# Optimization experiments

Hardware: AMD Instinct MI355X
Metric: run time of the kernel (lower is better)

Reference implementation:

```python
import jax, jax.numpy as jnp
import numpy as np

SHAPES = [(100, 100), (50, 50), (25, 25), (13, 13)]
EMBED, HEADS, LEVELS, POINTS = 256, 8, 4, 4
DH = EMBED // HEADS


def setup_inputs() -> dict:
    key = jax.random.key(0)
    ks = jax.random.split(key, 12)
    bs, nq = 4, 10000
    nv = sum(h * w for h, w in SHAPES)
    s = 0.02
    return {
        'query': jax.random.normal(ks[0], (bs, nq, EMBED), jnp.float32),
        'value': jax.random.normal(ks[1], (bs, nv, EMBED), jnp.float32),
        'reference_points': jax.random.uniform(ks[2], (bs, nq, LEVELS, 2), jnp.float32),
        'spatial_shapes': jnp.array(SHAPES, jnp.int32),
        'Wv': s * jax.random.normal(ks[3], (EMBED, EMBED), jnp.float32),
        'bv': jnp.zeros((EMBED,), jnp.float32),
        'Woff': s * jax.random.normal(ks[4], (EMBED, HEADS * LEVELS * POINTS * 2), jnp.float32),
        'boff': s * jax.random.normal(ks[5], (HEADS * LEVELS * POINTS * 2,), jnp.float32),
        'Ww': s * jax.random.normal(ks[6], (EMBED, HEADS * LEVELS * POINTS), jnp.float32),
        'bw': jnp.zeros((HEADS * LEVELS * POINTS,), jnp.float32),
        'Wo': s * jax.random.normal(ks[7], (EMBED, EMBED), jnp.float32),
        'bo': jnp.zeros((EMBED,), jnp.float32),
    }


def _msda(v, loc, aw, bs, nq):
    # v: (bs, nv, heads, dh); loc: (bs, nq, heads, L, P, 2) normalized in [0,1]
    # aw: (bs, nq, heads, L, P). Bilinear grid_sample, align_corners=False, zero padding.
    out = jnp.zeros((bs, HEADS, nq, DH), v.dtype)
    start = 0
    for l, (H, W) in enumerate(SHAPES):
        vl = v[:, start:start + H * W].transpose(0, 2, 1, 3)  # (bs, heads, H*W, dh)
        start += H * W
        locl = loc[:, :, :, l]                                # (bs, nq, heads, P, 2)
        x = locl[..., 0] * W - 0.5                            # align_corners=False mapping
        y = locl[..., 1] * H - 0.5
        x0 = jnp.floor(x); y0 = jnp.floor(y)
        fx = x - x0; fy = y - y0
        x0i = x0.astype(jnp.int32); y0i = y0.astype(jnp.int32)
        sampled = jnp.zeros((bs, HEADS, nq * POINTS, DH), v.dtype)
        for dy, wy in ((0, 1.0 - fy), (1, fy)):
            for dx, wx in ((0, 1.0 - fx), (1, fx)):
                xi = x0i + dx; yi = y0i + dy
                valid = (xi >= 0) & (xi < W) & (yi >= 0) & (yi < H)
                idx = jnp.clip(yi, 0, W and H - 1) * W + jnp.clip(xi, 0, W - 1)
                idx = jnp.clip(yi, 0, H - 1) * W + jnp.clip(xi, 0, W - 1)
                idx_t = idx.transpose(0, 2, 1, 3).reshape(bs, HEADS, nq * POINTS)
                g = jnp.take_along_axis(vl, idx_t[..., None], axis=2)  # (bs,heads,nq*P,dh)
                w = jnp.where(valid, wx * wy, 0.0).transpose(0, 2, 1, 3).reshape(bs, HEADS, -1)
                sampled = sampled + g * w[..., None]
        awl = aw[:, :, :, l].transpose(0, 2, 1, 3).reshape(bs, HEADS, nq * POINTS)
        out = out + (sampled * awl[..., None]).reshape(bs, HEADS, nq, POINTS, DH).sum(3)
    return out.transpose(0, 2, 1, 3).reshape(bs, nq, EMBED)


def reference(query, value, reference_points, spatial_shapes, Wv, bv, Woff, boff, Ww, bw, Wo, bo):
    bs, nq, _ = query.shape
    v = (value @ Wv + bv).reshape(bs, -1, HEADS, DH)
    off = (query @ Woff + boff).reshape(bs, nq, HEADS, LEVELS, POINTS, 2)
    aw = jax.nn.softmax((query @ Ww + bw).reshape(bs, nq, HEADS, LEVELS * POINTS), axis=-1)
    aw = aw.reshape(bs, nq, HEADS, LEVELS, POINTS)
    normalizer = jnp.stack([spatial_shapes[:, 1], spatial_shapes[:, 0]], -1).astype(query.dtype)  # (L,2) = (W,H)
    loc = reference_points[:, :, None, :, None, :] + off / normalizer[None, None, None, :, None, :]
    out = _msda(v, loc, aw, bs, nq)
    out = out @ Wo + bo
    return out + query  # identity residual (dropout in eval mode)
```

## Files before the change

### kernel.cpp

```cpp
#include <hip/hip_runtime.h>
#include <hip/hip_bf16.h>

#define BS     4
#define NQ     10000
#define NV     13294
#define EMBED  256
#define HEADS  8
#define LEVELS 4
#define POINTS 4
#define DH     32

typedef __attribute__((ext_vector_type(8))) short short8;
typedef __attribute__((ext_vector_type(4))) float floatx4;

static __device__ __forceinline__ unsigned short f2b(float f) {
    __hip_bfloat16 h = __float2bfloat16(f);
    return *(unsigned short*)&h;
}
static __device__ __forceinline__ float b2f(unsigned short u) {
    return __uint_as_float(((unsigned int)u) << 16);
}
static __device__ __forceinline__ unsigned int pk_bf16(float x, float y) {
    __hip_bfloat162 h = __float22bfloat162_rn(make_float2(x, y));
    unsigned int u; __builtin_memcpy(&u, &h, 4); return u;
}

__global__ __launch_bounds__(256) void prep_weights(
    const float* __restrict__ Wv,  const float* __restrict__ Woff,
    const float* __restrict__ boff,const float* __restrict__ Ww,
    const float* __restrict__ bw,  const float* __restrict__ Wo,
    unsigned short* __restrict__ Wvt, unsigned short* __restrict__ Wcatt,
    unsigned short* __restrict__ Wot, float* __restrict__ bcat)
{
    const int n = blockIdx.x;
    const int k = threadIdx.x;
    if (n < 256) {
        Wvt[n * 256 + k] = f2b(Wv[k * 256 + n]);
    } else if (n < 512) {
        Wcatt[(n - 256) * 256 + k] = f2b(Woff[k * 256 + (n - 256)]);
    } else if (n < 640) {
        Wcatt[(n - 256) * 256 + k] = f2b(Ww[k * 128 + (n - 512)]);
    } else {
        Wot[(n - 640) * 256 + k] = f2b(Wo[k * 256 + (n - 640)]);
    }
    if (n == 0) {
        for (int j = k; j < 384; j += 256)
            bcat[j] = (j < 256) ? boff[j] : bw[j - 256];
    }
}

#define ASTR 72

template<int MODE, bool AF32>
static __device__ __forceinline__ void gemm_body(
    unsigned short* As, unsigned short* Bsh,
    const void* __restrict__ Aptr, int M,
    const unsigned short* __restrict__ Bt,
    const float* __restrict__ bias,
    void* __restrict__ Cv, int ldc,
    const float* __restrict__ residual,
    int mb, int nb)
{
    const int t  = threadIdx.x;
    const int m0 = mb * 128;
    const int n0 = nb * 128;
    const int K  = 256;

    const int wv   = t >> 6;
    const int lane = t & 63;
    const int wm   = (wv & 1) * 64;
    const int wn   = (wv >> 1) * 64;
    const int lr   = lane & 15;
    const int lk   = (lane >> 4) * 8;

    floatx4 acc[4][4] = {};

    const int ar = t >> 1;
    const int ac = (t & 1) * 32;

    for (int k0 = 0; k0 < K; k0 += 64) {
        uint4 a[4] = {{}, {}, {}, {}};
        const int arow = m0 + ar;
        if (AF32) {
            if (arow < M) {
                const float4* s = (const float4*)((const float*)Aptr + (size_t)arow * K + k0 + ac);
                #pragma unroll
                for (int i = 0; i < 4; ++i) {
                    const float4 f0 = s[2 * i], f1 = s[2 * i + 1];
                    a[i].x = pk_bf16(f0.x, f0.y);
                    a[i].y = pk_bf16(f0.z, f0.w);
                    a[i].z = pk_bf16(f1.x, f1.y);
                    a[i].w = pk_bf16(f1.z, f1.w);
                }
            }
        } else {
            if (arow < M) {
                const uint4* s = (const uint4*)((const unsigned short*)Aptr + (size_t)arow * K + k0 + ac);
                a[0] = s[0]; a[1] = s[1]; a[2] = s[2]; a[3] = s[3];
            }
        }
        const uint4* bs = (const uint4*)(Bt + (size_t)(n0 + ar) * K + k0 + ac);
        const uint4 b0 = bs[0], b1 = bs[1], b2 = bs[2], b3 = bs[3];

        __syncthreads();
        {
            uint4* ad = (uint4*)&As[ar * ASTR + ac];
            ad[0] = a[0]; ad[1] = a[1]; ad[2] = a[2]; ad[3] = a[3];
            uint4* bd = (uint4*)&Bsh[ar * ASTR + ac];
            bd[0] = b0; bd[1] = b1; bd[2] = b2; bd[3] = b3;
        }
        __syncthreads();

        #pragma unroll
        for (int kk = 0; kk < 64; kk += 32) {
            short8 bf[4];
            #pragma unroll
            for (int nt = 0; nt < 4; ++nt)
                bf[nt] = *(const short8*)&Bsh[(wn + nt * 16 + lr) * ASTR + kk + lk];
            #pragma unroll
            for (int mt = 0; mt < 4; ++mt) {
                const short8 af = *(const short8*)&As[(wm + mt * 16 + lr) * ASTR + kk + lk];
                #pragma unroll
                for (int nt = 0; nt < 4; ++nt)
                    acc[mt][nt] = __builtin_amdgcn_mfma_f32_16x16x32_bf16(af, bf[nt], acc[mt][nt], 0, 0, 0);
            }
        }
    }

    const int rbase = m0 + wm + (lane >> 4) * 4;
    #pragma unroll
    for (int nt = 0; nt < 4; ++nt) {
        const int col = n0 + wn + nt * 16 + lr;
        const float bb = bias[col];
        #pragma unroll
        for (int mt = 0; mt < 4; ++mt) {
            #pragma unroll
            for (int r = 0; r < 4; ++r) {
                const int row = rbase + mt * 16 + r;
                if (row < M) {
                    float val = acc[mt][nt][r] + bb;
                    if (MODE == 2) val += residual[(size_t)row * ldc + col];
                    if (MODE == 0)
                        ((unsigned short*)Cv)[(size_t)row * ldc + col] = f2b(val);
                    else
                        ((float*)Cv)[(size_t)row * ldc + col] = val;
                }
            }
        }
    }
}

__global__ __launch_bounds__(256) void gemm_fused12(
    const float* __restrict__ value, const float* __restrict__ query,
    const unsigned short* __restrict__ Wvt, const unsigned short* __restrict__ Wcatt,
    const float* __restrict__ bv, const float* __restrict__ bcat,
    unsigned short* __restrict__ vout, unsigned short* __restrict__ projout)
{
    __shared__ __align__(16) unsigned short As[128 * ASTR];
    __shared__ __align__(16) unsigned short Bsh[128 * ASTR];
    const unsigned int bid = blockIdx.x;
    if (bid < 832u) {
        gemm_body<0, true>(As, Bsh, value, BS * NV, Wvt, bv, vout, 256, nullptr,
                           (int)(bid >> 1), (int)(bid & 1));
    } else {
        const unsigned int b2 = bid - 832u;
        gemm_body<0, true>(As, Bsh, query, BS * NQ, Wcatt, bcat, projout, 384, nullptr,
                           (int)(b2 / 3u), (int)(b2 % 3u));
    }
}

__global__ __launch_bounds__(256) void gemm_out(
    const unsigned short* __restrict__ msda, const unsigned short* __restrict__ Wot,
    const float* __restrict__ bo, float* __restrict__ out,
    const float* __restrict__ query)
{
    __shared__ __align__(16) unsigned short As[128 * ASTR];
    __shared__ __align__(16) unsigned short Bsh[128 * ASTR];
    gemm_body<2, false>(As, Bsh, msda, BS * NQ, Wot, bo, out, 256, query,
                        (int)blockIdx.x, (int)blockIdx.y);
}

__global__ __launch_bounds__(256) void msda_sample(
    const unsigned short* __restrict__ v,
    const unsigned short* __restrict__ proj,
    const float* __restrict__ rp,
    unsigned short* __restrict__ out)
{
    __shared__ __align__(16) unsigned int taps[4 * 1056];

    const int wave = threadIdx.x >> 6;
    const int lane = threadIdx.x & 63;
    const int q = blockIdx.x * 4 + wave;
    const int b = blockIdx.y;
    const int rowq = b * NQ + q;
    const unsigned short* prow = proj + (size_t)rowq * 384;

    const int hA = lane >> 3;
    const int li = lane & 7;
    const int c0 = li * 2;

    const ushort2 lgu = *(const ushort2*)&prow[256 + hA * 16 + c0];
    const float lgx = b2f(lgu.x), lgy = b2f(lgu.y);
    float mx = fmaxf(lgx, lgy);
    mx = fmaxf(mx, __shfl_xor(mx, 1));
    mx = fmaxf(mx, __shfl_xor(mx, 2));
    mx = fmaxf(mx, __shfl_xor(mx, 4));
    const float e0 = __expf(lgx - mx);
    const float e1 = __expf(lgy - mx);
    float ssum = e0 + e1;
    ssum += __shfl_xor(ssum, 1);
    ssum += __shfl_xor(ssum, 2);
    ssum += __shfl_xor(ssum, 4);
    const float inv = 1.0f / ssum;

    const int l = c0 >> 2;
    const int Wl = (l == 0) ? 100 : (l == 1) ? 50 : (l == 2) ? 25 : 13;
    const int st = (l == 0) ? 0 : (l == 1) ? 10000 : (l == 2) ? 12500 : 13125;
    const int Hl = Wl;
    const float fW = (float)Wl, fH = (float)Hl;

    const float2 rxy = *(const float2*)&rp[((size_t)rowq * 4 + l) * 2];

    unsigned int* tbase = taps + wave * 1056 + hA * 132;

    #pragma unroll
    for (int cc = 0; cc < 2; ++cc) {
        const int c = c0 + cc;
        const ushort2 oxyu = *(const ushort2*)&prow[hA * 32 + c * 2];
        const float ox = b2f(oxyu.x), oy = b2f(oxyu.y);
        const float aww = (cc ? e1 : e0) * inv;
        const float x = fmaf(rxy.x, fW, ox) - 0.5f;
        const float y = fmaf(rxy.y, fH, oy) - 0.5f;
        const float x0f = floorf(x), y0f = floorf(y);
        const float fx = x - x0f, fy = y - y0f;
        const int ix = (int)x0f, iy = (int)y0f;
        const float wxv[2] = {1.f - fx, fx};
        const float wyv[2] = {1.f - fy, fy};

        uint4 ent[2];
        #pragma unroll
        for (int tp = 0; tp < 4; ++tp) {
            const int dy = tp >> 1, dx = tp & 1;
            const int xi = ix + dx, yi = iy + dy;
            const bool ok = (xi >= 0) && (xi < Wl) && (yi >= 0) && (yi < Hl);
            const int cx = min(max(xi, 0), Wl - 1);
            const int cy = min(max(yi, 0), Hl - 1);
            const unsigned int off = (unsigned int)(st + cy * Wl + cx) * 512u + (unsigned int)hA * 64u;
            const float w = ok ? wyv[dy] * wxv[dx] * aww : 0.f;
            ((unsigned int*)&ent[tp >> 1])[(tp & 1) * 2 + 0] = off;
            ((unsigned int*)&ent[tp >> 1])[(tp & 1) * 2 + 1] = __float_as_uint(w);
        }
        *(uint4*)&tbase[(c * 4 + 0) * 2] = ent[0];
        *(uint4*)&tbase[(c * 4 + 2) * 2] = ent[1];
    }

    __syncthreads();

    const int h = lane >> 3;
    const unsigned int lane_off = (unsigned int)(lane & 7) * 8u;
    const char* vbase = (const char*)v + (size_t)b * NV * 512;
    const uint4* tp4 = (const uint4*)(taps + wave * 1056 + h * 132);

    float a0 = 0.f, a1 = 0.f, a2 = 0.f, a3 = 0.f;
    #pragma unroll 8
    for (int j = 0; j < 32; ++j) {
        const uint4 ee = tp4[j];
        const uint2 g0 = *(const uint2*)(vbase + (ee.x + lane_off));
        const uint2 g1 = *(const uint2*)(vbase + (ee.z + lane_off));
        const float w0 = __uint_as_float(ee.y);
        const float w1 = __uint_as_float(ee.w);
        a0 = fmaf(w0, __uint_as_float(g0.x << 16), a0);
        a1 = fmaf(w0, __uint_as_float(g0.x & 0xFFFF0000u), a1);
        a2 = fmaf(w0, __uint_as_float(g0.y << 16), a2);
        a3 = fmaf(w0, __uint_as_float(g0.y & 0xFFFF0000u), a3);
        a0 = fmaf(w1, __uint_as_float(g1.x << 16), a0);
        a1 = fmaf(w1, __uint_as_float(g1.x & 0xFFFF0000u), a1);
        a2 = fmaf(w1, __uint_as_float(g1.y << 16), a2);
        a3 = fmaf(w1, __uint_as_float(g1.y & 0xFFFF0000u), a3);
    }

    ushort4 o;
    o.x = f2b(a0); o.y = f2b(a1); o.z = f2b(a2); o.w = f2b(a3);
    *(ushort4*)&out[(size_t)rowq * 256 + h * 32 + (lane & 7) * 4] = o;
}

extern "C" void kernel_launch(void* const* d_in, const int* in_sizes, int n_in,
                              void* d_out, int out_size, void* d_ws, size_t ws_size,
                              hipStream_t stream) {
    const float* query = (const float*)d_in[0];
    const float* value = (const float*)d_in[1];
    const float* rp    = (const float*)d_in[2];
    const float* Wv    = (const float*)d_in[4];
    const float* bv    = (const float*)d_in[5];
    const float* Woff  = (const float*)d_in[6];
    const float* boff  = (const float*)d_in[7];
    const float* Ww    = (const float*)d_in[8];
    const float* bw    = (const float*)d_in[9];
    const float* Wo    = (const float*)d_in[10];
    const float* bo    = (const float*)d_in[11];
    float* out = (float*)d_out;

    const int Mv = BS * NV;
    const int Mq = BS * NQ;

    char* ws = (char*)d_ws;
    const size_t SZ_MSDA = (size_t)Mq * 256 * 2;
    const size_t SZ_V    = (size_t)Mv * 256 * 2;
    const size_t SZ_PROJ = (size_t)Mq * 384 * 2;
    unsigned short* msda  = (unsigned short*)(ws);
    unsigned short* v_bf  = (unsigned short*)(ws + SZ_MSDA);
    unsigned short* proj  = (unsigned short*)(ws + SZ_MSDA + SZ_V);
    char* wp = ws + SZ_MSDA + SZ_V + SZ_PROJ;
    unsigned short* Wvt   = (unsigned short*)(wp);
    unsigned short* Wcatt = (unsigned short*)(wp + 256 * 256 * 2);
    unsigned short* Wot   = (unsigned short*)(wp + 256 * 256 * 2 + 384 * 256 * 2);
    float*          bcat  = (float*)(wp + 256 * 256 * 2 + 384 * 256 * 2 + 256 * 256 * 2);

    prep_weights<<<896, 256, 0, stream>>>(Wv, Woff, boff, Ww, bw, Wo, Wvt, Wcatt, Wot, bcat);

    gemm_fused12<<<832 + 939, 256, 0, stream>>>(
        value, query, Wvt, Wcatt, bv, bcat, v_bf, proj);

    msda_sample<<<dim3(NQ / 4, BS), 256, 0, stream>>>(v_bf, proj, rp, msda);

    gemm_out<<<dim3((Mq + 127) / 128, 2), 256, 0, stream>>>(msda, Wot, bo, out, query);
}
```

Baseline: 332.7 us.

## Load GEMM operands directly from global memory into MFMA registers, dropping LDS staging

The GEMM body no longer stages A and B tiles through shared memory with barriers. Each wave now loads its MFMA fragments straight from global memory (converting fp32 A to bf16 in registers) and clamps out-of-range rows instead of zero-filling them. This removes LDS traffic and __syncthreads, which may raise occupancy. The cost is redundant global/L2 reads, since the two waves sharing a column range each reload B and the two sharing a row range each reload A, with less coalesced access.

After: 356.8 us. +7.2%, slower.

```diff
diff --git a/kernel.cpp b/kernel.cpp
--- a/kernel.cpp
+++ b/kernel.cpp
@@ -49,11 +49,8 @@
     }
 }
 
-#define ASTR 72
-
 template<int MODE, bool AF32>
-static __device__ __forceinline__ void gemm_body(
-    unsigned short* As, unsigned short* Bsh,
+static __device__ __forceinline__ void gemm_direct(
     const void* __restrict__ Aptr, int M,
     const unsigned short* __restrict__ Bt,
     const float* __restrict__ bias,
@@ -61,76 +58,57 @@
     const float* __restrict__ residual,
     int mb, int nb)
 {
-    const int t  = threadIdx.x;
-    const int m0 = mb * 128;
-    const int n0 = nb * 128;
-    const int K  = 256;
-
+    const int t    = threadIdx.x;
+    const int lane = t & 63;
     const int wv   = t >> 6;
-    const int lane = t & 63;
-    const int wm   = (wv & 1) * 64;
-    const int wn   = (wv >> 1) * 64;
+    const int wm   = mb * 128 + (wv & 1) * 64;
+    const int wn   = nb * 128 + (wv >> 1) * 64;
     const int lr   = lane & 15;
     const int lk   = (lane >> 4) * 8;
 
     floatx4 acc[4][4] = {};
 
-    const int ar = t >> 1;
-    const int ac = (t & 1) * 32;
-
-    for (int k0 = 0; k0 < K; k0 += 64) {
-        uint4 a[4] = {{}, {}, {}, {}};
-        const int arow = m0 + ar;
-        if (AF32) {
-            if (arow < M) {
-                const float4* s = (const float4*)((const float*)Aptr + (size_t)arow * K + k0 + ac);
-                #pragma unroll
-                for (int i = 0; i < 4; ++i) {
-                    const float4 f0 = s[2 * i], f1 = s[2 * i + 1];
-                    a[i].x = pk_bf16(f0.x, f0.y);
-                    a[i].y = pk_bf16(f0.z, f0.w);
-                    a[i].z = pk_bf16(f1.x, f1.y);
-                    a[i].w = pk_bf16(f1.z, f1.w);
-                }
-            }
-        } else {
-            if (arow < M) {
-                const uint4* s = (const uint4*)((const unsigned short*)Aptr + (size_t)arow * K + k0 + ac);
-                a[0] = s[0]; a[1] = s[1]; a[2] = s[2]; a[3] = s[3];
+    int arow[4];
+    #pragma unroll
+    for (int mt = 0; mt < 4; ++mt)
+        arow[mt] = min(wm + mt * 16 + lr, M - 1);
+
+    #pragma unroll 2
+    for (int k0 = 0; k0 < 256; k0 += 32) {
+        short8 bf[4];
+        #pragma unroll
+        for (int nt = 0; nt < 4; ++nt)
+            bf[nt] = *(const short8*)&Bt[(size_t)(wn + nt * 16 + lr) * 256 + k0 + lk];
+
+        short8 af[4];
+        #pragma unroll
+        for (int mt = 0; mt < 4; ++mt) {
+            if (AF32) {
+                const float4* s = (const float4*)((const float*)Aptr + (size_t)arow[mt] * 256 + k0 + lk);
+                const float4 f0 = s[0], f1 = s[1];
+                union { short8 v; unsigned int u[4]; } cv;
+                cv.u[0] = pk_bf16(f0.x, f0.y);
+                cv.u[1] = pk_bf16(f0.z, f0.w);
+                cv.u[2] = pk_bf16(f1.x, f1.y);
+                cv.u[3] = pk_bf16(f1.z, f1.w);
+                af[mt] = cv.v;
+            } else {
+                af[mt] = *(const short8*)&((const unsigned short*)Aptr)[(size_t)arow[mt] * 256 + k0 + lk];
             }
         }
-        const uint4* bs = (const uint4*)(Bt + (size_t)(n0 + ar) * K + k0 + ac);
-        const uint4 b0 = bs[0], b1 = bs[1], b2 = bs[2], b3 = bs[3];
-
-        __syncthreads();
-        {
-            uint4* ad = (uint4*)&As[ar * ASTR + ac];
-            ad[0] = a[0]; ad[1] = a[1]; ad[2] = a[2]; ad[3] = a[3];
-            uint4* bd = (uint4*)&Bsh[ar * ASTR + ac];
-            bd[0] = b0; bd[1] = b1; bd[2] = b2; bd[3] = b3;
-        }
-        __syncthreads();
-
-        #pragma unroll
-        for (int kk = 0; kk < 64; kk += 32) {
-            short8 bf[4];
+
+        #pragma unroll
+        for (int mt = 0; mt < 4; ++mt) {
             #pragma unroll
             for (int nt = 0; nt < 4; ++nt)
-                bf[nt] = *(const short8*)&Bsh[(wn + nt * 16 + lr) * ASTR + kk + lk];
-            #pragma unroll
-            for (int mt = 0; mt < 4; ++mt) {
-                const short8 af = *(const short8*)&As[(wm + mt * 16 + lr) * ASTR + kk + lk];
-                #pragma unroll
-                for (int nt = 0; nt < 4; ++nt)
-                    acc[mt][nt] = __builtin_amdgcn_mfma_f32_16x16x32_bf16(af, bf[nt], acc[mt][nt], 0, 0, 0);
-            }
+                acc[mt][nt] = __builtin_amdgcn_mfma_f32_16x16x32_bf16(af[mt], bf[nt], acc[mt][nt], 0, 0, 0);
         }
     }
 
-    const int rbase = m0 + wm + (lane >> 4) * 4;
+    const int rbase = wm + (lane >> 4) * 4;
     #pragma unroll
     for (int nt = 0; nt < 4; ++nt) {
-        const int col = n0 + wn + nt * 16 + lr;
+        const int col = wn + nt * 16 + lr;
         const float bb = bias[col];
         #pragma unroll
         for (int mt = 0; mt < 4; ++mt) {
@@ -156,16 +134,14 @@
     const float* __restrict__ bv, const float* __restrict__ bcat,
     unsigned short* __restrict__ vout, unsigned short* __restrict__ projout)
 {
-    __shared__ __align__(16) unsigned short As[128 * ASTR];
-    __shared__ __align__(16) unsigned short Bsh[128 * ASTR];
     const unsigned int bid = blockIdx.x;
     if (bid < 832u) {
-        gemm_body<0, true>(As, Bsh, value, BS * NV, Wvt, bv, vout, 256, nullptr,
-                           (int)(bid >> 1), (int)(bid & 1));
+        gemm_direct<0, true>(value, BS * NV, Wvt, bv, vout, 256, nullptr,
+                             (int)(bid >> 1), (int)(bid & 1));
     } else {
         const unsigned int b2 = bid - 832u;
-        gemm_body<0, true>(As, Bsh, query, BS * NQ, Wcatt, bcat, projout, 384, nullptr,
-                           (int)(b2 / 3u), (int)(b2 % 3u));
+        gemm_direct<0, true>(query, BS * NQ, Wcatt, bcat, projout, 384, nullptr,
+                             (int)(b2 / 3u), (int)(b2 % 3u));
     }
 }
 
@@ -174,10 +150,8 @@
     const float* __restrict__ bo, float* __restrict__ out,
     const float* __restrict__ query)
 {
-    __shared__ __align__(16) unsigned short As[128 * ASTR];
-    __shared__ __align__(16) unsigned short Bsh[128 * ASTR];
-    gemm_body<2, false>(As, Bsh, msda, BS * NQ, Wot, bo, out, 256, query,
-                        (int)blockIdx.x, (int)blockIdx.y);
+    gemm_direct<2, false>(msda, BS * NQ, Wot, bo, out, 256, query,
+                          (int)blockIdx.x, (int)blockIdx.y);
 }
 
 __global__ __launch_bounds__(256) void msda_sample(
@@ -300,8 +274,8 @@
     const float* bo    = (const float*)d_in[11];
     float* out = (float*)d_out;
 
+    const int Mq = BS * NQ;
     const int Mv = BS * NV;
-    const int Mq = BS * NQ;
 
     char* ws = (char*)d_ws;
     const size_t SZ_MSDA = (size_t)Mq * 256 * 2;
```

## Double-buffer GEMM B tiles via global_load_lds DMA with XOR swizzle and A prefetch

Applied to the files above, without the earlier changes.

Rewrites the GEMM main loop to prefetch the next K-slice: B weight tiles are loaded straight into a double-buffered LDS region with global_load_lds, and A rows are held in registers a step ahead. The B tile layout in LDS changes from padded rows to an XOR-swizzled chunk layout to avoid bank conflicts. The goal is to overlap global memory latency with MFMA work. The cost is more registers for the f32 A prefetch (8 float4) and more LDS, which may lower occupancy. The DMA loads are not followed by an explicit vmcnt wait before the barrier, so correctness depends on compiler-inserted waits.

New measurement: 345.4 us. 1.04x slower.

```diff
diff --git a/kernel.cpp b/kernel.cpp
--- a/kernel.cpp
+++ b/kernel.cpp
@@ -23,6 +23,12 @@
 static __device__ __forceinline__ unsigned int pk_bf16(float x, float y) {
     __hip_bfloat162 h = __float22bfloat162_rn(make_float2(x, y));
     unsigned int u; __builtin_memcpy(&u, &h, 4); return u;
+}
+static __device__ __forceinline__ void dma16(const unsigned short* g, unsigned short* l) {
+    __builtin_amdgcn_global_load_lds(
+        (const __attribute__((address_space(1))) unsigned int*)g,
+        (__attribute__((address_space(3))) unsigned int*)l,
+        16, 0, 0);
 }
 
 __global__ __launch_bounds__(256) void prep_weights(
@@ -64,7 +70,6 @@
     const int t  = threadIdx.x;
     const int m0 = mb * 128;
     const int n0 = nb * 128;
-    const int K  = 256;
 
     const int wv   = t >> 6;
     const int lane = t & 63;
@@ -73,50 +78,89 @@
     const int lr   = lane & 15;
     const int lk   = (lane >> 4) * 8;
 
-    floatx4 acc[4][4] = {};
-
     const int ar = t >> 1;
     const int ac = (t & 1) * 32;
-
-    for (int k0 = 0; k0 < K; k0 += 64) {
-        uint4 a[4] = {{}, {}, {}, {}};
-        const int arow = m0 + ar;
+    const bool arow_ok = (m0 + ar) < M;
+    const int brow_lo = lane >> 3;
+    const int bkcs    = lane & 7;
+
+    floatx4 acc[4][4] = {};
+    float4 a32[8];
+    uint4  a16[4];
+
+    {
         if (AF32) {
-            if (arow < M) {
-                const float4* s = (const float4*)((const float*)Aptr + (size_t)arow * K + k0 + ac);
-                #pragma unroll
-                for (int i = 0; i < 4; ++i) {
-                    const float4 f0 = s[2 * i], f1 = s[2 * i + 1];
-                    a[i].x = pk_bf16(f0.x, f0.y);
-                    a[i].y = pk_bf16(f0.z, f0.w);
-                    a[i].z = pk_bf16(f1.x, f1.y);
-                    a[i].w = pk_bf16(f1.z, f1.w);
-                }
-            }
+            const float4* s = (const float4*)((const float*)Aptr + (size_t)(m0 + ar) * 256 + ac);
+            #pragma unroll
+            for (int i = 0; i < 8; ++i) a32[i] = arow_ok ? s[i] : make_float4(0.f,0.f,0.f,0.f);
         } else {
-            if (arow < M) {
-                const uint4* s = (const uint4*)((const unsigned short*)Aptr + (size_t)arow * K + k0 + ac);
-                a[0] = s[0]; a[1] = s[1]; a[2] = s[2]; a[3] = s[3];
-            }
-        }
-        const uint4* bs = (const uint4*)(Bt + (size_t)(n0 + ar) * K + k0 + ac);
-        const uint4 b0 = bs[0], b1 = bs[1], b2 = bs[2], b3 = bs[3];
-
+            const uint4* s = (const uint4*)((const unsigned short*)Aptr + (size_t)(m0 + ar) * 256 + ac);
+            #pragma unroll
+            for (int i = 0; i < 4; ++i) a16[i] = arow_ok ? s[i] : make_uint4(0,0,0,0);
+        }
+        #pragma unroll
+        for (int j = 0; j < 4; ++j) {
+            const int row = (wv * 4 + j) * 8 + brow_lo;
+            const int kc  = bkcs ^ (row & 7);
+            dma16(Bt + (size_t)(n0 + row) * 256 + kc * 8,
+                  &Bsh[(((wv * 4 + j) * 64 + lane) * 8)]);
+        }
+    }
+
+    #pragma unroll
+    for (int it = 0; it < 4; ++it) {
+        const int buf = it & 1;
         __syncthreads();
         {
+            uint4 w[4];
+            if (AF32) {
+                #pragma unroll
+                for (int i = 0; i < 4; ++i) {
+                    w[i].x = pk_bf16(a32[2*i].x, a32[2*i].y);
+                    w[i].y = pk_bf16(a32[2*i].z, a32[2*i].w);
+                    w[i].z = pk_bf16(a32[2*i+1].x, a32[2*i+1].y);
+                    w[i].w = pk_bf16(a32[2*i+1].z, a32[2*i+1].w);
+                }
+            } else {
+                #pragma unroll
+                for (int i = 0; i < 4; ++i) w[i] = a16[i];
+            }
             uint4* ad = (uint4*)&As[ar * ASTR + ac];
-            ad[0] = a[0]; ad[1] = a[1]; ad[2] = a[2]; ad[3] = a[3];
-            uint4* bd = (uint4*)&Bsh[ar * ASTR + ac];
-            bd[0] = b0; bd[1] = b1; bd[2] = b2; bd[3] = b3;
+            ad[0] = w[0]; ad[1] = w[1]; ad[2] = w[2]; ad[3] = w[3];
         }
         __syncthreads();
 
+        if (it < 3) {
+            const int k0 = (it + 1) * 64;
+            if (AF32) {
+                const float4* s = (const float4*)((const float*)Aptr + (size_t)(m0 + ar) * 256 + k0 + ac);
+                #pragma unroll
+                for (int i = 0; i < 8; ++i) a32[i] = arow_ok ? s[i] : make_float4(0.f,0.f,0.f,0.f);
+            } else {
+                const uint4* s = (const uint4*)((const unsigned short*)Aptr + (size_t)(m0 + ar) * 256 + k0 + ac);
+                #pragma unroll
+                for (int i = 0; i < 4; ++i) a16[i] = arow_ok ? s[i] : make_uint4(0,0,0,0);
+            }
+            unsigned short* bdst = Bsh + (buf ^ 1) * (128 * 64);
+            #pragma unroll
+            for (int j = 0; j < 4; ++j) {
+                const int row = (wv * 4 + j) * 8 + brow_lo;
+                const int kc  = bkcs ^ (row & 7);
+                dma16(Bt + (size_t)(n0 + row) * 256 + k0 + kc * 8,
+                      &bdst[(((wv * 4 + j) * 64 + lane) * 8)]);
+            }
+        }
+
+        const unsigned short* bsrc = Bsh + buf * (128 * 64);
         #pragma unroll
         for (int kk = 0; kk < 64; kk += 32) {
+            const int kcl = (kk + lk) >> 3;
             short8 bf[4];
             #pragma unroll
-            for (int nt = 0; nt < 4; ++nt)
-                bf[nt] = *(const short8*)&Bsh[(wn + nt * 16 + lr) * ASTR + kk + lk];
+            for (int nt = 0; nt < 4; ++nt) {
+                const int n = wn + nt * 16 + lr;
+                bf[nt] = *(const short8*)&bsrc[(n * 8 + (kcl ^ (n & 7))) * 8];
+            }
             #pragma unroll
             for (int mt = 0; mt < 4; ++mt) {
                 const short8 af = *(const short8*)&As[(wm + mt * 16 + lr) * ASTR + kk + lk];
@@ -157,7 +201,7 @@
     unsigned short* __restrict__ vout, unsigned short* __restrict__ projout)
 {
     __shared__ __align__(16) unsigned short As[128 * ASTR];
-    __shared__ __align__(16) unsigned short Bsh[128 * ASTR];
+    __shared__ __align__(16) unsigned short Bsh[2 * 128 * 64];
     const unsigned int bid = blockIdx.x;
     if (bid < 832u) {
         gemm_body<0, true>(As, Bsh, value, BS * NV, Wvt, bv, vout, 256, nullptr,
@@ -175,7 +219,7 @@
     const float* __restrict__ query)
 {
     __shared__ __align__(16) unsigned short As[128 * ASTR];
-    __shared__ __align__(16) unsigned short Bsh[128 * ASTR];
+    __shared__ __align__(16) unsigned short Bsh[2 * 128 * 64];
     gemm_body<2, false>(As, Bsh, msda, BS * NQ, Wot, bo, out, 256, query,
                         (int)blockIdx.x, (int)blockIdx.y);
 }
@@ -300,8 +344,8 @@
     const float* bo    = (const float*)d_in[11];
     float* out = (float*)d_out;
 
+    const int Mq = BS * NQ;
     const int Mv = BS * NV;
-    const int Mq = BS * NQ;
 
     char* ws = (char*)d_ws;
     const size_t SZ_MSDA = (size_t)Mq * 256 * 2;
```
